# Optimization experiments

Hardware: AMD Instinct MI355X
Metric: run time of the kernel (lower is better)

Reference implementation:

```python
import jax, jax.numpy as jnp
import numpy as np


def setup_inputs() -> dict:
    key = jax.random.key(0)
    k1, k2, k3, k4 = jax.random.split(key, 4)
    T, H, I, E, K = 4096, 1024, 1024, 8, 2
    hidden_states = jax.random.normal(k1, (T, H), dtype=jnp.float32)
    router_logits = jax.random.normal(k2, (T, E), dtype=jnp.float32)
    # fused gate+up projection: [E, H, 2*I]; down projection: [E, I, H]
    up_weight = jax.random.normal(k3, (E, H, 2 * I), dtype=jnp.float32) * 0.02
    down_weight = jax.random.normal(k4, (E, I, H), dtype=jnp.float32) * 0.02
    return {"hidden_states": hidden_states, "router_logits": router_logits,
            "up_weight": up_weight, "down_weight": down_weight, "topk": K}


def reference(hidden_states, router_logits, up_weight, down_weight, topk):
    T, H = hidden_states.shape
    E = up_weight.shape[0]
    I = down_weight.shape[1]
    K = topk
    # select_experts: softmax over all experts, top-k, renormalize weights
    probs = jax.nn.softmax(router_logits, axis=-1)
    topk_w, topk_ids = jax.lax.top_k(probs, K)               # [T, K]
    topk_w = topk_w / jnp.sum(topk_w, axis=-1, keepdims=True)
    # expand tokens: each token is dispatched K times (grouped-GEMM operand)
    xk = jnp.repeat(hidden_states, K, axis=0)                # [T*K, H]
    flat_ids = topk_ids.reshape(-1)                          # [T*K]
    acc = jnp.zeros((T * K, H), dtype=hidden_states.dtype)
    for e in range(E):  # fixed small expert loop (grouped GEMM semantics)
        mask = (flat_ids == e).astype(hidden_states.dtype)[:, None]
        xe = xk * mask                                       # zero out non-e tokens
        gu = xe @ up_weight[e]                               # [T*K, 2I]
        h = jax.nn.silu(gu[:, :I]) * gu[:, I:]               # gated SiLU
        acc = acc + h @ down_weight[e]                       # [T*K, H]
    # combine: weighted sum over the K expert slots (reduce step)
    out = jnp.einsum('tk,tkh->th', topk_w, acc.reshape(T, K, H))
    return out
```

## Files before the change

### kernel.cpp

```cpp
#include <hip/hip_runtime.h>
#include <hip/hip_bf16.h>


#define T_TOK 4096
#define HDIM  1024
#define NEXP  8
#define RROWS (T_TOK * 2)
#define MAXPE T_TOK

typedef unsigned short u16;
typedef short v8s __attribute__((ext_vector_type(8)));
typedef float v4f __attribute__((ext_vector_type(4)));
typedef __attribute__((address_space(3))) unsigned int as3_u32;
typedef const __attribute__((address_space(1))) unsigned int as1_u32c;

__device__ __forceinline__ float b2f(u16 u) {
    union { unsigned int i; float f; } v; v.i = ((unsigned int)u) << 16; return v.f;
}
__device__ __forceinline__ u16 f2b(float f) {
    union { float f; unsigned int i; } v; v.f = f;
    unsigned int x = v.i;
    return (u16)((x + 0x7FFFu + ((x >> 16) & 1u)) >> 16);
}
__device__ __forceinline__ unsigned int pack2(float a, float b) {
    return (unsigned int)f2b(a) | ((unsigned int)f2b(b) << 16);
}
__device__ __forceinline__ void stage16(const u16* g, u16* l) {
    __builtin_amdgcn_global_load_lds((as1_u32c*)g, (as3_u32*)l, 16, 0, 0);
}

__global__ __launch_bounds__(256)
void prep_all(const float* __restrict__ X, const float* __restrict__ RL,
              const float* __restrict__ WU, const float* __restrict__ WD,
              u16* __restrict__ Xb, u16* __restrict__ WtU, u16* __restrict__ WtD,
              int* __restrict__ ids, float* __restrict__ wts,
              int* __restrict__ counts, int* __restrict__ rowbuf) {
    __shared__ __align__(16) u16 tile[64 * 72];
    const int bx = blockIdx.x;
    const int tid = threadIdx.x;

    if (bx < 6144) {
        int e = bx / 768;
        int r2 = bx - e * 768;
        int ky = r2 / 48;
        int bxx = r2 - ky * 48;
        const float* Wb; u16* Wtb; int N;
        if (bxx < 32) { Wb = WU + (size_t)e * 1024 * 2048; Wtb = WtU + (size_t)e * 2048 * 1024; N = 2048; }
        else          { Wb = WD + (size_t)e * 1024 * 1024; Wtb = WtD + (size_t)e * 1024 * 1024; N = 1024; bxx -= 32; }
        int n0 = bxx * 64, k0 = ky * 64;
        int r = tid >> 4, c4 = (tid & 15) * 4;
#pragma unroll
        for (int j = 0; j < 4; j++) {
            int k = r + j * 16;
            float4 f = *(const float4*)(Wb + (size_t)(k0 + k) * N + n0 + c4);
            tile[(c4 + 0) * 72 + k] = f2b(f.x);
            tile[(c4 + 1) * 72 + k] = f2b(f.y);
            tile[(c4 + 2) * 72 + k] = f2b(f.z);
            tile[(c4 + 3) * 72 + k] = f2b(f.w);
        }
        __syncthreads();
        int n = tid >> 2, kc = (tid & 3) * 16;
        uint4 v0 = *(const uint4*)&tile[n * 72 + kc];
        uint4 v1 = *(const uint4*)&tile[n * 72 + kc + 8];
        u16* dst = Wtb + (size_t)(n0 + n) * 1024 + k0 + kc;
        *(uint4*)dst = v0;
        *(uint4*)(dst + 8) = v1;
    } else if (bx < 10240) {
        int i = ((bx - 6144) * 256 + tid) * 4;
        float4 f = *(const float4*)(X + i);
        uint2 o; o.x = pack2(f.x, f.y); o.y = pack2(f.z, f.w);
        *(uint2*)(Xb + i) = o;
    } else {
        int t = (bx - 10240) * 256 + tid;
        float4 a = *(const float4*)(RL + t * NEXP);
        float4 b = *(const float4*)(RL + t * NEXP + 4);
        float l[NEXP] = {a.x, a.y, a.z, a.w, b.x, b.y, b.z, b.w};
        int i0 = 0;
#pragma unroll
        for (int q = 1; q < NEXP; q++) if (l[q] > l[i0]) i0 = q;
        int i1 = (i0 == 0) ? 1 : 0;
#pragma unroll
        for (int q = 0; q < NEXP; q++) if (q != i0 && l[q] > l[i1]) i1 = q;
        float w0 = 1.0f / (1.0f + expf(l[i1] - l[i0]));
        ids[2 * t] = i0;     ids[2 * t + 1] = i1;
        wts[2 * t] = w0;     wts[2 * t + 1] = 1.0f - w0;
        int p0 = atomicAdd(&counts[i0], 1);
        rowbuf[i0 * MAXPE + p0] = 2 * t;
        int p1 = atomicAdd(&counts[i1], 1);
        rowbuf[i1 * MAXPE + p1] = 2 * t + 1;
    }
}

template<int PHASE>
__global__ __launch_bounds__(256)
void mfma_gemm(const u16* __restrict__ A, const u16* __restrict__ Bt,
               u16* __restrict__ H,
               const int* __restrict__ counts, const int* __restrict__ rowbuf) {
    const int bi = blockIdx.x;
    const int xcd = bi & 7, kb = bi >> 3;
    int e, ct, rt;
    if (PHASE == 1) { int p = (kb & 15) * 8 + xcd; e = p >> 4; ct = p & 15; rt = kb >> 4; }
    else            { int p = (kb & 7) * 8 + xcd;  e = p >> 3; ct = p & 7;  rt = kb >> 3; }
    const int cnt = counts[e];
    if (rt * 128 >= cnt) return;
    const int tid = threadIdx.x;
    const int lane = tid & 63, wave = tid >> 6;

    __shared__ __align__(16) u16 sA[128 * 64];
    __shared__ __align__(16) u16 sB[128 * 64];
    __shared__ int srid[128];

    if (tid < 128) {
        int idx = rt * 128 + tid;
        srid[tid] = (idx < cnt) ? rowbuf[e * MAXPE + idx] : -1;
    }
    __syncthreads();

    const int lrow = lane >> 3;
    const int lchunk = (lane & 7) ^ lrow;
    const u16* aPtr[4]; const u16* bPtr[4];
    u16 *aDst[4], *bDst[4];
#pragma unroll
    for (int p = 0; p < 4; p++) {
        int region = p * 4 + wave;
        int r = region * 8 + lrow;
        int rid = srid[r];
        int arow = (rid < 0) ? 0 : (PHASE == 1 ? (rid >> 1) : rid);
        aPtr[p] = A + (size_t)arow * 1024 + lchunk * 8;
        aDst[p] = sA + region * 512 + lane * 8;
        int n;
        if (PHASE == 1) n = (r < 64) ? (ct * 64 + r) : (1024 + ct * 64 + (r - 64));
        else            n = ct * 128 + r;
        bPtr[p] = Bt + (size_t)e * (PHASE == 1 ? 2048 : 1024) * 1024
                     + (size_t)n * 1024 + lchunk * 8;
        bDst[p] = sB + region * 512 + lane * 8;
    }

    const int quad = lane >> 4, mr = lane & 15;
    const int swA = mr & 7;
    const v4f zf = {0.f, 0.f, 0.f, 0.f};
    v4f acc[2][8];
#pragma unroll
    for (int i = 0; i < 2; i++)
#pragma unroll
        for (int j = 0; j < 8; j++) acc[i][j] = zf;

    for (int kk = 0; kk < 16; kk++) {
        __syncthreads();
#pragma unroll
        for (int p = 0; p < 4; p++) {
            stage16(aPtr[p] + kk * 64, aDst[p]);
            stage16(bPtr[p] + kk * 64, bDst[p]);
        }
        __syncthreads();
#pragma unroll
        for (int kh = 0; kh < 2; kh++) {
            const int c = kh * 4 + quad;
            v8s a0 = *(const v8s*)(sA + (wave * 32 + mr) * 64 + ((c ^ swA) * 8));
            v8s a1 = *(const v8s*)(sA + (wave * 32 + 16 + mr) * 64 + ((c ^ swA) * 8));
#pragma unroll
            for (int nf = 0; nf < 8; nf++) {
                v8s b = *(const v8s*)(sB + (nf * 16 + mr) * 64 + ((c ^ swA) * 8));
                acc[0][nf] = __builtin_amdgcn_mfma_f32_16x16x32_bf16(a0, b, acc[0][nf], 0, 0, 0);
                acc[1][nf] = __builtin_amdgcn_mfma_f32_16x16x32_bf16(a1, b, acc[1][nf], 0, 0, 0);
            }
        }
    }

#pragma unroll
    for (int mf = 0; mf < 2; mf++) {
#pragma unroll
        for (int reg = 0; reg < 4; reg++) {
            int rl = wave * 32 + mf * 16 + quad * 4 + reg;
            int grow = srid[rl];
            if (grow < 0) continue;
            if (PHASE == 1) {
                size_t base = (size_t)grow * 1024 + ct * 64 + mr;
#pragma unroll
                for (int nf = 0; nf < 4; nf++) {
                    float g = acc[mf][nf][reg], u = acc[mf][nf + 4][reg];
                    H[base + nf * 16] = f2b((g / (1.0f + expf(-g))) * u);
                }
            } else {
                size_t base = (size_t)grow * 1024 + ct * 128 + mr;
#pragma unroll
                for (int nf = 0; nf < 8; nf++)
                    H[base + nf * 16] = f2b(acc[mf][nf][reg]);
            }
        }
    }
}

__global__ void combine_kernel(const u16* __restrict__ accb,
                               const float* __restrict__ wts,
                               float* __restrict__ out) {
    int g = blockIdx.x * blockDim.x + threadIdx.x;
    int t = g >> 8;
    int c = (g & 255) * 4;
    float w0 = wts[2 * t], w1 = wts[2 * t + 1];
    ushort4 a = *(const ushort4*)(accb + (size_t)(2 * t) * 1024 + c);
    ushort4 b = *(const ushort4*)(accb + (size_t)(2 * t + 1) * 1024 + c);
    float4 o;
    o.x = w0 * b2f(a.x) + w1 * b2f(b.x);
    o.y = w0 * b2f(a.y) + w1 * b2f(b.y);
    o.z = w0 * b2f(a.z) + w1 * b2f(b.z);
    o.w = w0 * b2f(a.w) + w1 * b2f(b.w);
    *(float4*)(out + (size_t)t * 1024 + c) = o;
}

__global__ void router_kernel(const float* __restrict__ logits,
                              int* __restrict__ ids, float* __restrict__ wts) {
    int t = blockIdx.x * blockDim.x + threadIdx.x;
    if (t >= T_TOK) return;
    float4 a = *(const float4*)(logits + t * NEXP);
    float4 b = *(const float4*)(logits + t * NEXP + 4);
    float l[NEXP] = {a.x, a.y, a.z, a.w, b.x, b.y, b.z, b.w};
    int i0 = 0;
#pragma unroll
    for (int i = 1; i < NEXP; i++) if (l[i] > l[i0]) i0 = i;
    int i1 = (i0 == 0) ? 1 : 0;
#pragma unroll
    for (int i = 0; i < NEXP; i++) if (i != i0 && l[i] > l[i1]) i1 = i;
    float w0 = 1.0f / (1.0f + expf(l[i1] - l[i0]));
    ids[2 * t] = i0;     ids[2 * t + 1] = i1;
    wts[2 * t] = w0;     wts[2 * t + 1] = 1.0f - w0;
}

__global__ void bucket_kernel(const int* __restrict__ ids,
                              int* __restrict__ counts, int* __restrict__ rowbuf) {
    int r = blockIdx.x * blockDim.x + threadIdx.x;
    if (r >= RROWS) return;
    int e = ids[r];
    int pos = atomicAdd(&counts[e], 1);
    rowbuf[e * MAXPE + pos] = r;
}

template<int GATED, int AF32>
__global__ __launch_bounds__(256)
void moe_gemm_kernel(const void* __restrict__ Av,
                     const float* __restrict__ B,
                     u16* __restrict__ C,
                     const int* __restrict__ counts,
                     const int* __restrict__ rowbuf,
                     int rowShift, int NB) {
    const int e   = blockIdx.z;
    const int cnt = counts[e];
    const int rt  = blockIdx.y;
    if (rt * 128 >= cnt) return;
    const int ct  = blockIdx.x;
    const int tid = threadIdx.x;

    __shared__ __align__(16) u16 sA[128 * 40];
    __shared__ __align__(16) u16 sB[(GATED ? 2 : 1) * 64 * 40];
    __shared__ int srid[128];

    if (tid < 128) {
        int idx = rt * 128 + tid;
        srid[tid] = (idx < cnt) ? rowbuf[e * MAXPE + idx] : -1;
    }
    __syncthreads();

    const int ar = tid >> 1, ac = (tid & 1) * 16;
    int arid = srid[ar];
    const float* aSrcF = 0; const u16* aSrcH = 0;
    if (arid >= 0) {
        if (AF32) aSrcF = (const float*)Av + (size_t)(arid >> rowShift) * HDIM + ac;
        else      aSrcH = (const u16*)Av + (size_t)(arid >> rowShift) * HDIM + ac;
    }
    u16* aDst = sA + ar * 40 + ac;

    const int kq2 = (tid >> 4) * 2, n4 = (tid & 15) * 4;
    const float* bSrcG = B + (size_t)e * 1024 * NB + (size_t)kq2 * NB + ct * 64 + n4;
    const float* bSrcU = bSrcG + 1024;

    const int lane = tid & 63, wave = tid >> 6;
    const int quad = lane >> 4, mr = lane & 15;

    const v4f zf = {0.f, 0.f, 0.f, 0.f};
    v4f accG[2][4], accU[2][4];
#pragma unroll
    for (int i = 0; i < 2; i++)
#pragma unroll
        for (int j = 0; j < 4; j++) { accG[i][j] = zf; accU[i][j] = zf; }

    for (int kk = 0; kk < HDIM / 32; kk++) {
        uint4 aw0 = make_uint4(0, 0, 0, 0), aw1 = make_uint4(0, 0, 0, 0);
        if (AF32) {
            if (aSrcF) {
                float4 f0 = *(const float4*)(aSrcF + kk * 32);
                float4 f1 = *(const float4*)(aSrcF + kk * 32 + 4);
                float4 f2 = *(const float4*)(aSrcF + kk * 32 + 8);
                float4 f3 = *(const float4*)(aSrcF + kk * 32 + 12);
                aw0 = make_uint4(pack2(f0.x, f0.y), pack2(f0.z, f0.w),
                                 pack2(f1.x, f1.y), pack2(f1.z, f1.w));
                aw1 = make_uint4(pack2(f2.x, f2.y), pack2(f2.z, f2.w),
                                 pack2(f3.x, f3.y), pack2(f3.z, f3.w));
            }
        } else {
            if (aSrcH) {
                aw0 = *(const uint4*)(aSrcH + kk * 32);
                aw1 = *(const uint4*)(aSrcH + kk * 32 + 8);
            }
        }
        const size_t bOff = (size_t)kk * 32 * NB;
        float4 g0 = *(const float4*)(bSrcG + bOff);
        float4 g1 = *(const float4*)(bSrcG + bOff + NB);
        float4 u0 = make_float4(0, 0, 0, 0), u1 = make_float4(0, 0, 0, 0);
        if (GATED) {
            u0 = *(const float4*)(bSrcU + bOff);
            u1 = *(const float4*)(bSrcU + bOff + NB);
        }

        __syncthreads();
        *(uint4*)aDst = aw0;
        *(uint4*)(aDst + 8) = aw1;
        {
            const float gx[4] = {g0.x, g0.y, g0.z, g0.w};
            const float gy[4] = {g1.x, g1.y, g1.z, g1.w};
#pragma unroll
            for (int j = 0; j < 4; j++)
                *(unsigned int*)&sB[(n4 + j) * 40 + kq2] = pack2(gx[j], gy[j]);
            if (GATED) {
                const float ux[4] = {u0.x, u0.y, u0.z, u0.w};
                const float uy[4] = {u1.x, u1.y, u1.z, u1.w};
#pragma unroll
                for (int j = 0; j < 4; j++)
                    *(unsigned int*)&sB[64 * 40 + (n4 + j) * 40 + kq2] = pack2(ux[j], uy[j]);
            }
        }
        __syncthreads();

        v8s af0 = *(const v8s*)(sA + (wave * 32 + mr) * 40 + quad * 8);
        v8s af1 = *(const v8s*)(sA + (wave * 32 + 16 + mr) * 40 + quad * 8);
#pragma unroll
        for (int nf = 0; nf < 4; nf++) {
            v8s bg = *(const v8s*)(sB + (nf * 16 + mr) * 40 + quad * 8);
            accG[0][nf] = __builtin_amdgcn_mfma_f32_16x16x32_bf16(af0, bg, accG[0][nf], 0, 0, 0);
            accG[1][nf] = __builtin_amdgcn_mfma_f32_16x16x32_bf16(af1, bg, accG[1][nf], 0, 0, 0);
            if (GATED) {
                v8s bu = *(const v8s*)(sB + 64 * 40 + (nf * 16 + mr) * 40 + quad * 8);
                accU[0][nf] = __builtin_amdgcn_mfma_f32_16x16x32_bf16(af0, bu, accU[0][nf], 0, 0, 0);
                accU[1][nf] = __builtin_amdgcn_mfma_f32_16x16x32_bf16(af1, bu, accU[1][nf], 0, 0, 0);
            }
        }
    }

#pragma unroll
    for (int mf = 0; mf < 2; mf++) {
#pragma unroll
        for (int reg = 0; reg < 4; reg++) {
            int rl = wave * 32 + mf * 16 + quad * 4 + reg;
            int grow = srid[rl];
            if (grow < 0) continue;
            size_t base = (size_t)grow * 1024 + ct * 64 + mr;
#pragma unroll
            for (int nf = 0; nf < 4; nf++) {
                float g = accG[mf][nf][reg];
                float val;
                if (GATED) {
                    float u = accU[mf][nf][reg];
                    val = (g / (1.0f + expf(-g))) * u;
                } else {
                    val = g;
                }
                C[base + nf * 16] = f2b(val);
            }
        }
    }
}

extern "C" void kernel_launch(void* const* d_in, const int* in_sizes, int n_in,
                              void* d_out, int out_size, void* d_ws, size_t ws_size,
                              hipStream_t stream) {
    const float *X = 0, *RL = 0, *WU = 0, *WD = 0;
    for (int i = 0; i < n_in; i++) {
        switch (in_sizes[i]) {
            case T_TOK * HDIM:        X  = (const float*)d_in[i]; break;
            case T_TOK * NEXP:        RL = (const float*)d_in[i]; break;
            case NEXP * HDIM * 2048:  WU = (const float*)d_in[i]; break;
            case NEXP * HDIM * 1024:  WD = (const float*)d_in[i]; break;
            default: break;
        }
    }
    if (!X)  X  = (const float*)d_in[0];
    if (!RL) RL = (const float*)d_in[1];
    if (!WU) WU = (const float*)d_in[2];
    if (!WD) WD = (const float*)d_in[3];
    float* OUT = (float*)d_out;

    char* ws = (char*)d_ws;
    int*   ids    = (int*)(ws + 0);
    float* wts    = (float*)(ws + 32768);
    int*   counts = (int*)(ws + 65536);
    int*   rowbuf = (int*)(ws + 65792);
    u16* Xb   = (u16*)(ws + 196864);
    u16* WtU  = (u16*)(ws + 8585472);
    u16* WtD  = (u16*)(ws + 42139904);
    u16* HbufF= (u16*)(ws + 58917120);
    u16* AccF = WtU;
    const size_t needFast = 75694336ull;
    u16* Hbuf = (u16*)(ws + 196864);
    u16* Acc  = (u16*)(ws + 196864 + 16777216);

    hipMemsetAsync(counts, 0, NEXP * sizeof(int), stream);

    if (ws_size >= needFast) {
        prep_all<<<10256, 256, 0, stream>>>(
            X, RL, WU, WD, Xb, WtU, WtD, ids, wts, counts, rowbuf);
        mfma_gemm<1><<<4096, 256, 0, stream>>>(Xb, WtU, HbufF, counts, rowbuf);
        mfma_gemm<2><<<2048, 256, 0, stream>>>(HbufF, WtD, AccF, counts, rowbuf);
        combine_kernel<<<T_TOK, 256, 0, stream>>>(AccF, wts, OUT);
    } else {
        router_kernel<<<T_TOK / 256, 256, 0, stream>>>(RL, ids, wts);
        bucket_kernel<<<RROWS / 256, 256, 0, stream>>>(ids, counts, rowbuf);
        moe_gemm_kernel<1, 1><<<dim3(16, 32, NEXP), 256, 0, stream>>>(
            (const void*)X, WU, Hbuf, counts, rowbuf, 1, 2048);
        moe_gemm_kernel<0, 0><<<dim3(16, 32, NEXP), 256, 0, stream>>>(
            (const void*)Hbuf, WD, Acc, counts, rowbuf, 0, 1024);
        combine_kernel<<<T_TOK, 256, 0, stream>>>(Acc, wts, OUT);
    }
}
```

Baseline: 265.0 us.

## Move down-weight conversion into first GEMM launch and enlarge transpose tiles

```diff
diff --git a/kernel.cpp b/kernel.cpp
--- a/kernel.cpp
+++ b/kernel.cpp
@@ -29,49 +29,68 @@
     __builtin_amdgcn_global_load_lds((as1_u32c*)g, (as3_u32*)l, 16, 0, 0);
 }
 
+__device__ __forceinline__ void cvt_tile(const float* __restrict__ Wb,
+                                         u16* __restrict__ Wtb,
+                                         int N, int n0b, int k0b, u16* sm) {
+    const int tid = threadIdx.x;
+    const int m = tid & 15, rr = tid >> 4;
+    float4 f[16];
+#pragma unroll
+    for (int s = 0; s < 4; s++)
+#pragma unroll
+        for (int j = 0; j < 4; j++)
+            f[s * 4 + j] = *(const float4*)(Wb + (size_t)(k0b + s * 64 + rr * 4 + j) * N
+                                               + n0b + m * 4);
+#pragma unroll
+    for (int s = 0; s < 4; s++) {
+        const int kc = s * 16 + rr;
+        const float* fp = (const float*)&f[s * 4];
+#pragma unroll
+        for (int nl = 0; nl < 4; nl++) {
+            int n_l = m * 4 + nl;
+            uint2 v;
+            v.x = pack2(fp[nl], fp[4 + nl]);
+            v.y = pack2(fp[8 + nl], fp[12 + nl]);
+            *(uint2*)&sm[n_l * 256 + ((kc ^ (n_l & 15)) << 2)] = v;
+        }
+    }
+    __syncthreads();
+    const int n_l = tid >> 2, q = tid & 3, sw = n_l & 15;
+    u16* dst = Wtb + (size_t)(n0b + n_l) * 1024 + k0b + q * 64;
+#pragma unroll
+    for (int c2 = 0; c2 < 8; c2++) {
+        uint2 a = *(const uint2*)&sm[n_l * 256 + (((q * 16 + 2 * c2) ^ sw) << 2)];
+        uint2 b = *(const uint2*)&sm[n_l * 256 + (((q * 16 + 2 * c2 + 1) ^ sw) << 2)];
+        uint4 o; o.x = a.x; o.y = a.y; o.z = b.x; o.w = b.y;
+        *(uint4*)(dst + c2 * 8) = o;
+    }
+}
+
 __global__ __launch_bounds__(256)
 void prep_all(const float* __restrict__ X, const float* __restrict__ RL,
-              const float* __restrict__ WU, const float* __restrict__ WD,
-              u16* __restrict__ Xb, u16* __restrict__ WtU, u16* __restrict__ WtD,
+              const float* __restrict__ WU,
+              u16* __restrict__ Xb, u16* __restrict__ WtU,
               int* __restrict__ ids, float* __restrict__ wts,
               int* __restrict__ counts, int* __restrict__ rowbuf) {
-    __shared__ __align__(16) u16 tile[64 * 72];
+    __shared__ __align__(16) u16 sm[64 * 256];
     const int bx = blockIdx.x;
     const int tid = threadIdx.x;
 
-    if (bx < 6144) {
-        int e = bx / 768;
-        int r2 = bx - e * 768;
-        int ky = r2 / 48;
-        int bxx = r2 - ky * 48;
-        const float* Wb; u16* Wtb; int N;
-        if (bxx < 32) { Wb = WU + (size_t)e * 1024 * 2048; Wtb = WtU + (size_t)e * 2048 * 1024; N = 2048; }
-        else          { Wb = WD + (size_t)e * 1024 * 1024; Wtb = WtD + (size_t)e * 1024 * 1024; N = 1024; bxx -= 32; }
-        int n0 = bxx * 64, k0 = ky * 64;
-        int r = tid >> 4, c4 = (tid & 15) * 4;
-#pragma unroll
-        for (int j = 0; j < 4; j++) {
-            int k = r + j * 16;
-            float4 f = *(const float4*)(Wb + (size_t)(k0 + k) * N + n0 + c4);
-            tile[(c4 + 0) * 72 + k] = f2b(f.x);
-            tile[(c4 + 1) * 72 + k] = f2b(f.y);
-            tile[(c4 + 2) * 72 + k] = f2b(f.z);
-            tile[(c4 + 3) * 72 + k] = f2b(f.w);
-        }
-        __syncthreads();
-        int n = tid >> 2, kc = (tid & 3) * 16;
-        uint4 v0 = *(const uint4*)&tile[n * 72 + kc];
-        uint4 v1 = *(const uint4*)&tile[n * 72 + kc + 8];
-        u16* dst = Wtb + (size_t)(n0 + n) * 1024 + k0 + kc;
-        *(uint4*)dst = v0;
-        *(uint4*)(dst + 8) = v1;
-    } else if (bx < 10240) {
-        int i = ((bx - 6144) * 256 + tid) * 4;
-        float4 f = *(const float4*)(X + i);
-        uint2 o; o.x = pack2(f.x, f.y); o.y = pack2(f.z, f.w);
-        *(uint2*)(Xb + i) = o;
+    if (bx < 1024) {
+        int e = bx >> 7, r = bx & 127;
+        int nt = r >> 2, kt = r & 3;
+        cvt_tile(WU + (size_t)e * 1024 * 2048, WtU + (size_t)e * 2048 * 1024,
+                 2048, nt * 64, kt * 256, sm);
+    } else if (bx < 1536) {
+        int base = (bx - 1024) * 8192 + tid * 4;
+#pragma unroll
+        for (int j = 0; j < 8; j++) {
+            float4 fx = *(const float4*)(X + base + j * 1024);
+            uint2 o; o.x = pack2(fx.x, fx.y); o.y = pack2(fx.z, fx.w);
+            *(uint2*)(Xb + base + j * 1024) = o;
+        }
     } else {
-        int t = (bx - 10240) * 256 + tid;
+        int t = (bx - 1536) * 256 + tid;
         float4 a = *(const float4*)(RL + t * NEXP);
         float4 b = *(const float4*)(RL + t * NEXP + 4);
         float l[NEXP] = {a.x, a.y, a.z, a.w, b.x, b.y, b.z, b.w};
@@ -95,8 +114,21 @@
 __global__ __launch_bounds__(256)
 void mfma_gemm(const u16* __restrict__ A, const u16* __restrict__ Bt,
                u16* __restrict__ H,
-               const int* __restrict__ counts, const int* __restrict__ rowbuf) {
-    const int bi = blockIdx.x;
+               const int* __restrict__ counts, const int* __restrict__ rowbuf,
+               const float* __restrict__ WD, u16* __restrict__ WtD) {
+    __shared__ __align__(16) u16 smem[128 * 64 * 2];
+    __shared__ int srid[128];
+    const int bi0 = blockIdx.x;
+
+    if (PHASE == 1 && bi0 < 512) {
+        int e = bi0 >> 6, r = bi0 & 63;
+        int nt = r >> 2, kt = r & 3;
+        cvt_tile(WD + (size_t)e * 1024 * 1024, WtD + (size_t)e * 1024 * 1024,
+                 1024, nt * 64, kt * 256, smem);
+        return;
+    }
+
+    const int bi = (PHASE == 1) ? bi0 - 512 : bi0;
     const int xcd = bi & 7, kb = bi >> 3;
     int e, ct, rt;
     if (PHASE == 1) { int p = (kb & 15) * 8 + xcd; e = p >> 4; ct = p & 15; rt = kb >> 4; }
@@ -106,9 +138,8 @@
     const int tid = threadIdx.x;
     const int lane = tid & 63, wave = tid >> 6;
 
-    __shared__ __align__(16) u16 sA[128 * 64];
-    __shared__ __align__(16) u16 sB[128 * 64];
-    __shared__ int srid[128];
+    u16* sA = smem;
+    u16* sB = smem + 128 * 64;
 
     if (tid < 128) {
         int idx = rt * 128 + tid;
@@ -405,10 +436,11 @@
     hipMemsetAsync(counts, 0, NEXP * sizeof(int), stream);
 
     if (ws_size >= needFast) {
-        prep_all<<<10256, 256, 0, stream>>>(
-            X, RL, WU, WD, Xb, WtU, WtD, ids, wts, counts, rowbuf);
-        mfma_gemm<1><<<4096, 256, 0, stream>>>(Xb, WtU, HbufF, counts, rowbuf);
-        mfma_gemm<2><<<2048, 256, 0, stream>>>(HbufF, WtD, AccF, counts, rowbuf);
+        prep_all<<<1552, 256, 0, stream>>>(
+            X, RL, WU, Xb, WtU, ids, wts, counts, rowbuf);
+        mfma_gemm<1><<<4608, 256, 0, stream>>>(Xb, WtU, HbufF, counts, rowbuf, WD, WtD);
+        mfma_gemm<2><<<2048, 256, 0, stream>>>(HbufF, WtD, AccF, counts, rowbuf,
+                                               (const float*)0, (u16*)0);
         combine_kernel<<<T_TOK, 256, 0, stream>>>(AccF, wts, OUT);
     } else {
         router_kernel<<<T_TOK / 256, 256, 0, stream>>>(RL, ids, wts);
```

Measured after the change: 268.9 us. Within noise of the previous version (+1.5%).
